# Kernel tuning notes

Hardware: AMD Instinct MI355X
Metric: run time of the kernel (lower is better)

The kernel has to match this reference:

```python
import jax, jax.numpy as jnp
import numpy as np

IN_F = 128
OUT_F = 128
SCALE = float(np.sqrt(OUT_F))

def swish(x):
    return x * jax.nn.sigmoid(x)

def setup_inputs() -> dict:
    key = jax.random.key(0)
    ks = jax.random.split(key, 10)
    B, A = 4, 4096
    s = 1.0 / np.sqrt(IN_F)
    return {
        "x": jax.random.normal(ks[0], (B, A, IN_F), dtype=jnp.float32),
        "connectivity": jax.random.normal(ks[1], (B, A, A), dtype=jnp.float32),
        "Wq": jax.random.uniform(ks[2], (IN_F, OUT_F), jnp.float32, -s, s),
        "Wk": jax.random.uniform(ks[3], (IN_F, OUT_F), jnp.float32, -s, s),
        "Wv": jax.random.uniform(ks[4], (IN_F, OUT_F), jnp.float32, -s, s),
        "W1": jax.random.uniform(ks[5], (OUT_F, OUT_F), jnp.float32, -s, s),
        "b1": jnp.zeros((OUT_F,), jnp.float32),
        "W2": jax.random.uniform(ks[6], (OUT_F, OUT_F), jnp.float32, -s, s),
        "b2": jnp.zeros((OUT_F,), jnp.float32),
        "gamma": jnp.ones((OUT_F,), jnp.float32),
        "beta": jnp.zeros((OUT_F,), jnp.float32),
    }

def reference(x, connectivity, Wq, Wk, Wv, W1, b1, W2, b2, gamma, beta):
    # Q,K,V projections (no bias): [B,A,D]
    Q = jnp.einsum('bah,hd->bad', x, Wq)
    K = jnp.einsum('bah,hd->bad', x, Wk)
    V = jnp.einsum('bah,hd->bad', x, Wv)
    # dense all-pairs scores with additive connectivity bias: [B,A,A]
    scores = jnp.einsum('bqd,bkd->bqk', Q, K) / SCALE + connectivity
    alpha = jax.nn.softmax(scores, axis=-1)
    # dropout p=0.0 / eval mode -> identity
    H = jnp.einsum('bqk,bkd->bqd', alpha, V)
    # Swish-MLP tail
    h = swish(H)
    h = h @ W1 + b1
    h = swish(h)
    h = h @ W2 + b2
    # LayerNorm over last dim (eps=1e-5 as torch default)
    mu = jnp.mean(h, axis=-1, keepdims=True)
    var = jnp.var(h, axis=-1, keepdims=True)
    return (h - mu) * jax.lax.rsqrt(var + 1e-5) * gamma + beta
```

## Files before the change

### kernel.cpp

```cpp
#include <hip/hip_runtime.h>

#define L2E 1.44269504088896340736f
#define INV_SCALE 0.08838834764831845f

typedef _Float16 half8 __attribute__((ext_vector_type(8)));
typedef _Float16 half4 __attribute__((ext_vector_type(4)));
typedef float f32x4 __attribute__((ext_vector_type(4)));

__device__ __forceinline__ float exp2_fast(float x) {
#if __has_builtin(__builtin_amdgcn_exp2f)
  return __builtin_amdgcn_exp2f(x);
#else
  return exp2f(x);
#endif
}

__device__ __forceinline__ f32x4 mfma16(half8 a, half8 b, f32x4 c) {
  return __builtin_amdgcn_mfma_f32_16x16x32_f16(a, b, c, 0, 0, 0);
}

__device__ __forceinline__ void gload16(const void* g, void* l) {
  __builtin_amdgcn_global_load_lds(
      (const __attribute__((address_space(1))) void*)g,
      (__attribute__((address_space(3))) void*)l, 16, 0, 0);
}

__device__ __forceinline__ float swish_f(float v) {
  return v / (1.f + exp2_fast(-L2E * v));
}

template <int CTRL>
__device__ __forceinline__ float dppmov(float x) {
  int xi = __builtin_bit_cast(int, x);
  int r = __builtin_amdgcn_update_dpp(xi, xi, CTRL, 0xf, 0xf, false);
  return __builtin_bit_cast(float, r);
}
__device__ __forceinline__ float red16_sum(float x) {
  x += dppmov<0xB1>(x);
  x += dppmov<0x4E>(x);
  x += dppmov<0x141>(x);
  x += dppmov<0x140>(x);
  return x;
}

__global__ __launch_bounds__(256) void prep_kernel(
    const float* __restrict__ Wq, const float* __restrict__ Wk,
    const float* __restrict__ Wv, const float* __restrict__ W1,
    const float* __restrict__ W2, _Float16* __restrict__ Wf) {
  const int g = blockIdx.x * 256 + threadIdx.x;
  const int mat = g >> 11, rem = g & 2047;
  const int f = rem >> 6, lane = rem & 63;
  const int n = (f >> 2) * 16 + (lane & 15);
  const int k0 = (f & 3) * 32 + (lane >> 4) * 8;
  const float* W = (mat == 0) ? Wq : (mat == 1) ? Wk : (mat == 2) ? Wv
                   : (mat == 3) ? W1 : W2;
  half8 h;
#pragma unroll
  for (int j = 0; j < 8; ++j) h[j] = (_Float16)W[(k0 + j) * 128 + n];
  *(half8*)(Wf + (size_t)g * 8) = h;
}

__global__ __launch_bounds__(256) void kv_kernel(
    const float* __restrict__ x, const _Float16* __restrict__ Wf,
    _Float16* __restrict__ Kg, _Float16* __restrict__ Vg) {
  __shared__ __align__(16) _Float16 sc[64 * 136];
  const int tid = threadIdx.x;
  const int w = tid >> 6, lane = tid & 63;
  const int n16 = lane & 15, quad = lane >> 4;
  const int blk = blockIdx.x;

  half8 xf[4];
  {
    const float* xr = x + (size_t)(blk * 64 + w * 16 + n16) * 128 + quad * 8;
#pragma unroll
    for (int kc = 0; kc < 4; ++kc) {
      float4 a = *(const float4*)(xr + kc * 32);
      float4 b = *(const float4*)(xr + kc * 32 + 4);
      half8 h;
      h[0] = (_Float16)a.x; h[1] = (_Float16)a.y;
      h[2] = (_Float16)a.z; h[3] = (_Float16)a.w;
      h[4] = (_Float16)b.x; h[5] = (_Float16)b.y;
      h[6] = (_Float16)b.z; h[7] = (_Float16)b.w;
      xf[kc] = h;
    }
  }

  for (int mat = 0; mat < 2; ++mat) {
    f32x4 acc[8];
#pragma unroll
    for (int ct = 0; ct < 8; ++ct) acc[ct] = f32x4{0.f, 0.f, 0.f, 0.f};
#pragma unroll
    for (int ct = 0; ct < 8; ++ct)
#pragma unroll
      for (int kc = 0; kc < 4; ++kc) {
        half8 wf = *(const half8*)(Wf +
            ((size_t)((mat + 1) * 32 + ct * 4 + kc) * 64 + lane) * 8);
        acc[ct] = mfma16(xf[kc], wf, acc[ct]);
      }
#pragma unroll
    for (int ct = 0; ct < 8; ++ct)
#pragma unroll
      for (int r = 0; r < 4; ++r)
        sc[(w * 16 + quad * 4 + r) * 136 + ct * 16 + n16] = (_Float16)acc[ct][r];
    __syncthreads();

    if (mat == 0) {
#pragma unroll
      for (int i = 0; i < 4; ++i) {
        const int c = tid + 256 * i;
        const int ln = c & 63, kc = (c >> 6) & 3, ct = (c >> 8) & 1, tl = (c >> 9) & 1;
        half8 v = *(const half8*)&sc[(tl * 32 + ct * 16 + (ln & 15)) * 136 +
                                     kc * 32 + (ln >> 4) * 8];
        *(half8*)(Kg + ((((size_t)(blk * 2 + tl)) * 2 + ct) * 4 + kc) * 512 + ln * 8) = v;
      }
    } else {
#pragma unroll
      for (int i = 0; i < 4; ++i) {
        const int c = tid + 256 * i;
        const int ln = c & 63, dt = (c >> 6) & 7, tl = (c >> 9) & 1;
        const int q2 = ln >> 4, nn = ln & 15;
        half8 v;
#pragma unroll
        for (int j = 0; j < 8; ++j)
          v[j] = sc[(tl * 32 + q2 * 8 + j) * 136 + dt * 16 + nn];
        *(half8*)(Vg + (((size_t)(blk * 2 + tl)) * 8 + dt) * 512 + ln * 8) = v;
      }
    }
    __syncthreads();
  }
}

__global__ __launch_bounds__(128) void flash_kernel(
    const float* __restrict__ x, const float* __restrict__ conn,
    const _Float16* __restrict__ Wf,
    const _Float16* __restrict__ Kg, const _Float16* __restrict__ Vg,
    _Float16* __restrict__ Og, float2* __restrict__ Ml,
    int nsplit, int nt) {
  __shared__ __align__(16) _Float16 kb[2][4096];
  __shared__ __align__(16) _Float16 vb[2][4096];
  __shared__ __align__(16) _Float16 pb[2][656];
  __shared__ __align__(16) float alb[2][16];

  const int tid = threadIdx.x, w = tid >> 6, lane = tid & 63;
  const int n16 = lane & 15, quad = lane >> 4;
  const int bid = blockIdx.x;
  int batch, sk, rg;
  if (nsplit == 2) {
    batch = bid & 3; sk = (bid >> 2) & 1; rg = bid >> 3;
  } else {
    batch = bid & 3; sk = 0; rg = bid >> 2;
  }
  const int rt_g = batch * 256 + rg * 2 + w;
  const int t0 = sk * nt;

  half8 qf[4];
  {
    half8 xf[4];
    const float* xr = x + (size_t)(batch * 4096 + rg * 32 + w * 16 + n16) * 128 + quad * 8;
#pragma unroll
    for (int kc = 0; kc < 4; ++kc) {
      float4 a = *(const float4*)(xr + kc * 32);
      float4 b = *(const float4*)(xr + kc * 32 + 4);
      half8 h;
      h[0] = (_Float16)a.x; h[1] = (_Float16)a.y;
      h[2] = (_Float16)a.z; h[3] = (_Float16)a.w;
      h[4] = (_Float16)b.x; h[5] = (_Float16)b.y;
      h[6] = (_Float16)b.z; h[7] = (_Float16)b.w;
      xf[kc] = h;
    }
    _Float16* tw = &kb[w][0];
#pragma unroll
    for (int ct = 0; ct < 8; ++ct) {
      f32x4 aq = f32x4{0.f, 0.f, 0.f, 0.f};
#pragma unroll
      for (int kc = 0; kc < 4; ++kc) {
        half8 wf = *(const half8*)(Wf + ((size_t)(ct * 4 + kc) * 64 + lane) * 8);
        aq = mfma16(xf[kc], wf, aq);
      }
#pragma unroll
      for (int r = 0; r < 4; ++r)
        tw[(quad * 4 + r) * 136 + ct * 16 + n16] = (_Float16)aq[r];
    }
#pragma unroll
    for (int kc = 0; kc < 4; ++kc)
      qf[kc] = *(const half8*)(tw + n16 * 136 + kc * 32 + quad * 8);
  }
  __syncthreads();

  const _Float16* kp = Kg + (size_t)batch * 524288 + (size_t)t0 * 4096 + tid * 8;
  const _Float16* vp = Vg + (size_t)batch * 524288 + (size_t)t0 * 4096 + tid * 8;
  const float* cp = conn + (size_t)batch * 16777216 +
                    (size_t)(rg * 32 + w * 16 + n16) * 4096 +
                    (size_t)t0 * 32 + quad * 4;
  const int wbase = (tid & ~63) * 8;

  auto stage = [&](int t, int buf) {
    const _Float16* ks = kp + (size_t)t * 4096;
    const _Float16* vs = vp + (size_t)t * 4096;
#pragma unroll
    for (int c = 0; c < 4; ++c) {
      gload16(ks + c * 1024, &kb[buf][c * 1024 + wbase]);
      gload16(vs + c * 1024, &vb[buf][c * 1024 + wbase]);
    }
  };
  auto ldconn = [&](int i, float4* cr) {
    const float* c0 = cp + (size_t)i * 32;
    cr[0] = *(const float4*)c0;
    cr[1] = *(const float4*)(c0 + 16);
  };

  f32x4 o[8];
#pragma unroll
  for (int dt = 0; dt < 8; ++dt) o[dt] = f32x4{0.f, 0.f, 0.f, 0.f};
  float m_i = -__builtin_inff();
  float l_i = 0.f;

  float4 ca[2], cb[2];
  stage(0, 0);
  ldconn(0, ca);
  __syncthreads();

  auto compute = [&](int buf, const float4* cc) {
    f32x4 s0 = f32x4{0.f, 0.f, 0.f, 0.f};
    f32x4 s1 = f32x4{0.f, 0.f, 0.f, 0.f};
    const _Float16* kc_ = kb[buf];
#pragma unroll
    for (int kc = 0; kc < 4; ++kc) {
      half8 kf0 = *(const half8*)&kc_[kc * 512 + lane * 8];
      half8 kf1 = *(const half8*)&kc_[(4 + kc) * 512 + lane * 8];
      s0 = mfma16(kf0, qf[kc], s0);
      s1 = mfma16(kf1, qf[kc], s1);
    }
    float pr[8];
#pragma unroll
    for (int r = 0; r < 4; ++r) {
      pr[r] = fmaf(s0[r], INV_SCALE, cc[0][r]);
      pr[4 + r] = fmaf(s1[r], INV_SCALE, cc[1][r]);
    }
    float mx = pr[0];
#pragma unroll
    for (int c = 1; c < 8; ++c) mx = fmaxf(mx, pr[c]);
    mx = fmaxf(mx, __shfl_xor(mx, 16, 64));
    mx = fmaxf(mx, __shfl_xor(mx, 32, 64));
    if (__any(mx > m_i)) {
      const float mn = fmaxf(m_i, mx);
      const float al = exp2_fast((m_i - mn) * L2E);
      m_i = mn;
      l_i *= al;
      if (quad == 0) alb[w][n16] = al;
      const float4 av = *(const float4*)&alb[w][quad * 4];
#pragma unroll
      for (int dt = 0; dt < 8; ++dt)
#pragma unroll
        for (int r = 0; r < 4; ++r) o[dt][r] *= av[r];
    }
    const float nm = -m_i * L2E;
#pragma unroll
    for (int c = 0; c < 8; ++c) pr[c] = exp2_fast(fmaf(pr[c], L2E, nm));
    float sm = pr[0];
#pragma unroll
    for (int c = 1; c < 8; ++c) sm += pr[c];
    sm += __shfl_xor(sm, 16, 64);
    sm += __shfl_xor(sm, 32, 64);
    l_i += sm;
    _Float16* pw = pb[w];
    half4 p0, p1;
#pragma unroll
    for (int r = 0; r < 4; ++r) {
      p0[r] = (_Float16)pr[r];
      p1[r] = (_Float16)pr[4 + r];
    }
    *(half4*)(pw + n16 * 40 + quad * 4) = p0;
    *(half4*)(pw + n16 * 40 + 16 + quad * 4) = p1;
    half8 pf = *(const half8*)(pw + n16 * 40 + quad * 8);
    const _Float16* vc = vb[buf];
#pragma unroll
    for (int dt = 0; dt < 8; ++dt) {
      half8 vf = *(const half8*)&vc[dt * 512 + lane * 8];
      o[dt] = mfma16(pf, vf, o[dt]);
    }
  };

#pragma unroll 1
  for (int i = 0; i < nt; i += 2) {
    stage(i + 1, 1);
    ldconn(i + 1, cb);
    compute(0, ca);
    __syncthreads();
    if (i + 2 < nt) {
      stage(i + 2, 0);
      ldconn(i + 2, ca);
    }
    compute(1, cb);
    __syncthreads();
  }

  if (quad == 0) alb[w][n16] = l_i;
  const float4 lv = *(const float4*)&alb[w][quad * 4];
  float il[4];
#pragma unroll
  for (int r = 0; r < 4; ++r) il[r] = 1.f / lv[r];
  _Float16* tw = &kb[w][0];
#pragma unroll
  for (int dt = 0; dt < 8; ++dt)
#pragma unroll
    for (int r = 0; r < 4; ++r)
      tw[(quad * 4 + r) * 136 + dt * 16 + n16] = (_Float16)(o[dt][r] * il[r]);
  _Float16* ob = Og + ((size_t)(sk * 1024 + rt_g) * 4) * 512;
#pragma unroll
  for (int kc = 0; kc < 4; ++kc) {
    half8 of = *(const half8*)(tw + n16 * 136 + kc * 32 + quad * 8);
    *(half8*)(ob + kc * 512 + lane * 8) = of;
  }
  if (quad == 0)
    Ml[sk * 16384 + rt_g * 16 + n16] = make_float2(m_i, l_i);
}

__global__ __launch_bounds__(256) void mlp_kernel(
    const _Float16* __restrict__ Og, const float2* __restrict__ Ml,
    const _Float16* __restrict__ Wf,
    const float* __restrict__ b1, const float* __restrict__ b2,
    const float* __restrict__ gamma, const float* __restrict__ beta,
    float* __restrict__ out, int nsplit) {
  __shared__ __align__(16) _Float16 hb[4][2176];
  const int tid = threadIdx.x, w = tid >> 6, lane = tid & 63;
  const int n16 = lane & 15, quad = lane >> 4;
  const int rt_g = blockIdx.x * 4 + w;

  float2 ml[2];
  float m = -__builtin_inff();
  for (int s = 0; s < nsplit; ++s) {
    ml[s] = Ml[s * 16384 + rt_g * 16 + n16];
    m = fmaxf(m, ml[s].x);
  }
  float wgt[2], wsum = 0.f;
  for (int s = 0; s < nsplit; ++s) {
    wgt[s] = ml[s].y * exp2_fast((ml[s].x - m) * L2E);
    wsum += wgt[s];
  }
  const float inv = 1.f / wsum;

  half8 hf[4];
#pragma unroll
  for (int kc = 0; kc < 4; ++kc) {
    float hv[8] = {0, 0, 0, 0, 0, 0, 0, 0};
    for (int s = 0; s < nsplit; ++s) {
      half8 ofr = *(const half8*)(Og +
          ((size_t)(s * 1024 + rt_g) * 4 + kc) * 512 + lane * 8);
#pragma unroll
      for (int j = 0; j < 8; ++j) hv[j] += wgt[s] * (float)ofr[j];
    }
    half8 h;
#pragma unroll
    for (int j = 0; j < 8; ++j) h[j] = (_Float16)swish_f(hv[j] * inv);
    hf[kc] = h;
  }

  float b1v[8], b2v[8], gv[8], bv[8];
#pragma unroll
  for (int ct = 0; ct < 8; ++ct) {
    b1v[ct] = b1[ct * 16 + n16];
    b2v[ct] = b2[ct * 16 + n16];
    gv[ct] = gamma[ct * 16 + n16];
    bv[ct] = beta[ct * 16 + n16];
  }

  f32x4 acc[8];
#pragma unroll
  for (int ct = 0; ct < 8; ++ct) acc[ct] = f32x4{0.f, 0.f, 0.f, 0.f};
#pragma unroll
  for (int ct = 0; ct < 8; ++ct)
#pragma unroll
    for (int kc = 0; kc < 4; ++kc) {
      half8 wf = *(const half8*)(Wf +
          ((size_t)(3 * 32 + ct * 4 + kc) * 64 + lane) * 8);
      acc[ct] = mfma16(hf[kc], wf, acc[ct]);
    }
  _Float16* hw = hb[w];
#pragma unroll
  for (int ct = 0; ct < 8; ++ct)
#pragma unroll
    for (int r = 0; r < 4; ++r)
      hw[(quad * 4 + r) * 136 + ct * 16 + n16] =
          (_Float16)swish_f(acc[ct][r] + b1v[ct]);
  half8 h1f[4];
#pragma unroll
  for (int kc = 0; kc < 4; ++kc)
    h1f[kc] = *(const half8*)(hw + n16 * 136 + kc * 32 + quad * 8);

#pragma unroll
  for (int ct = 0; ct < 8; ++ct) acc[ct] = f32x4{0.f, 0.f, 0.f, 0.f};
#pragma unroll
  for (int ct = 0; ct < 8; ++ct)
#pragma unroll
    for (int kc = 0; kc < 4; ++kc) {
      half8 wf = *(const half8*)(Wf +
          ((size_t)(4 * 32 + ct * 4 + kc) * 64 + lane) * 8);
      acc[ct] = mfma16(h1f[kc], wf, acc[ct]);
    }
  float hx[8][4];
  float sm[4] = {0, 0, 0, 0}, ss[4] = {0, 0, 0, 0};
#pragma unroll
  for (int ct = 0; ct < 8; ++ct)
#pragma unroll
    for (int r = 0; r < 4; ++r) {
      const float v = acc[ct][r] + b2v[ct];
      hx[ct][r] = v;
      sm[r] += v;
      ss[r] += v * v;
    }
#pragma unroll
  for (int r = 0; r < 4; ++r) {
    sm[r] = red16_sum(sm[r]);
    ss[r] = red16_sum(ss[r]);
  }
#pragma unroll
  for (int r = 0; r < 4; ++r) {
    const float mu = sm[r] * (1.f / 128.f);
    const float var = ss[r] * (1.f / 128.f) - mu * mu;
    const float rstd = rsqrtf(var + 1e-5f);
    const size_t row = (size_t)rt_g * 16 + quad * 4 + r;
#pragma unroll
    for (int ct = 0; ct < 8; ++ct)
      out[row * 128 + ct * 16 + n16] = (hx[ct][r] - mu) * rstd * gv[ct] + bv[ct];
  }
}

extern "C" void kernel_launch(void* const* d_in, const int* in_sizes, int n_in,
                              void* d_out, int out_size, void* d_ws,
                              size_t ws_size, hipStream_t stream) {
  const float* x     = (const float*)d_in[0];
  const float* conn  = (const float*)d_in[1];
  const float* Wq    = (const float*)d_in[2];
  const float* Wk    = (const float*)d_in[3];
  const float* Wv    = (const float*)d_in[4];
  const float* W1    = (const float*)d_in[5];
  const float* b1    = (const float*)d_in[6];
  const float* W2    = (const float*)d_in[7];
  const float* b2    = (const float*)d_in[8];
  const float* gamma = (const float*)d_in[9];
  const float* beta  = (const float*)d_in[10];
  float* out = (float*)d_out;

  const size_t need2 =
      ((size_t)81920 + 4 * 2097152) * 2 + 2 * 16384 * sizeof(float2);
  const int nsplit = (ws_size >= need2) ? 2 : 1;
  const int nt = 128 / nsplit;

  _Float16* Wf = (_Float16*)d_ws;
  _Float16* Kg = Wf + 81920;
  _Float16* Vg = Kg + 2097152;
  _Float16* Og = Vg + 2097152;
  float2* Ml = (float2*)(Og + (size_t)2097152 * nsplit);

  prep_kernel<<<40, 256, 0, stream>>>(Wq, Wk, Wv, W1, W2, Wf);
  kv_kernel<<<256, 256, 0, stream>>>(x, Wf, Kg, Vg);
  flash_kernel<<<512 * nsplit, 128, 0, stream>>>(x, conn, Wf, Kg, Vg, Og, Ml,
                                                 nsplit, nt);
  mlp_kernel<<<256, 256, 0, stream>>>(Og, Ml, Wf, b1, b2, gamma, beta, out,
                                      nsplit);
}
```

Baseline: 459.8 us.

## Template flash kernel on wave count, use four-wave blocks with four-way KV split

The flash attention kernel is templated on the number of waves per block. With enough workspace it launches 4-wave (256-thread) blocks that cover 64 query rows and share each staged K/V tile, and splits the key range four ways. Each K/V tile loaded into LDS is now reused by twice as many rows, cutting redundant K/V traffic per row, while the four-way split keeps the grid at 1024 blocks. The cost is more partial output written to workspace and merged in the MLP kernel, plus larger blocks that may lower occupancy.

```diff
diff --git a/kernel.cpp b/kernel.cpp
--- a/kernel.cpp
+++ b/kernel.cpp
@@ -130,7 +130,8 @@
   }
 }
 
-__global__ __launch_bounds__(128) void flash_kernel(
+template <int NW>
+__global__ __launch_bounds__(NW * 64) void flash_kernel(
     const float* __restrict__ x, const float* __restrict__ conn,
     const _Float16* __restrict__ Wf,
     const _Float16* __restrict__ Kg, const _Float16* __restrict__ Vg,
@@ -138,25 +139,30 @@
     int nsplit, int nt) {
   __shared__ __align__(16) _Float16 kb[2][4096];
   __shared__ __align__(16) _Float16 vb[2][4096];
-  __shared__ __align__(16) _Float16 pb[2][656];
-  __shared__ __align__(16) float alb[2][16];
+  __shared__ __align__(16) _Float16 pb[NW][656];
+  __shared__ __align__(16) float alb[NW][16];
 
   const int tid = threadIdx.x, w = tid >> 6, lane = tid & 63;
   const int n16 = lane & 15, quad = lane >> 4;
   const int bid = blockIdx.x;
   int batch, sk, rg;
-  if (nsplit == 2) {
+  if (nsplit == 4) {
+    batch = bid & 3; sk = (bid >> 2) & 3; rg = bid >> 4;
+  } else if (nsplit == 2) {
     batch = bid & 3; sk = (bid >> 2) & 1; rg = bid >> 3;
   } else {
     batch = bid & 3; sk = 0; rg = bid >> 2;
   }
-  const int rt_g = batch * 256 + rg * 2 + w;
+  const int rt_g = batch * 256 + rg * NW + w;
   const int t0 = sk * nt;
+  const int rowb = rg * (NW * 16) + w * 16 + n16;
+
+  _Float16* scratch = (w < 2) ? &kb[w][0] : &vb[w - 2][0];
 
   half8 qf[4];
   {
     half8 xf[4];
-    const float* xr = x + (size_t)(batch * 4096 + rg * 32 + w * 16 + n16) * 128 + quad * 8;
+    const float* xr = x + ((size_t)batch * 4096 + rowb) * 128 + quad * 8;
 #pragma unroll
     for (int kc = 0; kc < 4; ++kc) {
       float4 a = *(const float4*)(xr + kc * 32);
@@ -168,7 +174,7 @@
       h[6] = (_Float16)b.z; h[7] = (_Float16)b.w;
       xf[kc] = h;
     }
-    _Float16* tw = &kb[w][0];
+    _Float16* tw = scratch;
 #pragma unroll
     for (int ct = 0; ct < 8; ++ct) {
       f32x4 aq = f32x4{0.f, 0.f, 0.f, 0.f};
@@ -189,18 +195,18 @@
 
   const _Float16* kp = Kg + (size_t)batch * 524288 + (size_t)t0 * 4096 + tid * 8;
   const _Float16* vp = Vg + (size_t)batch * 524288 + (size_t)t0 * 4096 + tid * 8;
-  const float* cp = conn + (size_t)batch * 16777216 +
-                    (size_t)(rg * 32 + w * 16 + n16) * 4096 +
+  const float* cp = conn + (size_t)batch * 16777216 + (size_t)rowb * 4096 +
                     (size_t)t0 * 32 + quad * 4;
   const int wbase = (tid & ~63) * 8;
+  constexpr int NC = 8 / NW;
 
   auto stage = [&](int t, int buf) {
     const _Float16* ks = kp + (size_t)t * 4096;
     const _Float16* vs = vp + (size_t)t * 4096;
 #pragma unroll
-    for (int c = 0; c < 4; ++c) {
-      gload16(ks + c * 1024, &kb[buf][c * 1024 + wbase]);
-      gload16(vs + c * 1024, &vb[buf][c * 1024 + wbase]);
+    for (int c = 0; c < NC; ++c) {
+      gload16(ks + c * (NW * 512), &kb[buf][c * (NW * 512) + wbase]);
+      gload16(vs + c * (NW * 512), &vb[buf][c * (NW * 512) + wbase]);
     }
   };
   auto ldconn = [&](int i, float4* cr) {
@@ -300,7 +306,7 @@
   float il[4];
 #pragma unroll
   for (int r = 0; r < 4; ++r) il[r] = 1.f / lv[r];
-  _Float16* tw = &kb[w][0];
+  _Float16* tw = scratch;
 #pragma unroll
   for (int dt = 0; dt < 8; ++dt)
 #pragma unroll
@@ -327,13 +333,13 @@
   const int n16 = lane & 15, quad = lane >> 4;
   const int rt_g = blockIdx.x * 4 + w;
 
-  float2 ml[2];
+  float2 ml[4];
   float m = -__builtin_inff();
   for (int s = 0; s < nsplit; ++s) {
     ml[s] = Ml[s * 16384 + rt_g * 16 + n16];
     m = fmaxf(m, ml[s].x);
   }
-  float wgt[2], wsum = 0.f;
+  float wgt[4], wsum = 0.f;
   for (int s = 0; s < nsplit; ++s) {
     wgt[s] = ml[s].y * exp2_fast((ml[s].x - m) * L2E);
     wsum += wgt[s];
@@ -442,9 +448,12 @@
   const float* beta  = (const float*)d_in[10];
   float* out = (float*)d_out;
 
+  const size_t baseElems = (size_t)81920 + 2 * 2097152;
+  const size_t need4 =
+      (baseElems + 4 * 2097152) * 2 + 4 * 16384 * sizeof(float2);
   const size_t need2 =
-      ((size_t)81920 + 4 * 2097152) * 2 + 2 * 16384 * sizeof(float2);
-  const int nsplit = (ws_size >= need2) ? 2 : 1;
+      (baseElems + 2 * 2097152) * 2 + 2 * 16384 * sizeof(float2);
+  const int nsplit = (ws_size >= need4) ? 4 : (ws_size >= need2) ? 2 : 1;
   const int nt = 128 / nsplit;
 
   _Float16* Wf = (_Float16*)d_ws;
@@ -455,8 +464,16 @@
 
   prep_kernel<<<40, 256, 0, stream>>>(Wq, Wk, Wv, W1, W2, Wf);
   kv_kernel<<<256, 256, 0, stream>>>(x, Wf, Kg, Vg);
-  flash_kernel<<<512 * nsplit, 128, 0, stream>>>(x, conn, Wf, Kg, Vg, Og, Ml,
-                                                 nsplit, nt);
+  if (nsplit == 4) {
+    flash_kernel<4><<<1024, 256, 0, stream>>>(x, conn, Wf, Kg, Vg, Og, Ml,
+                                              nsplit, nt);
+  } else if (nsplit == 2) {
+    flash_kernel<2><<<1024, 128, 0, stream>>>(x, conn, Wf, Kg, Vg, Og, Ml,
+                                              nsplit, nt);
+  } else {
+    flash_kernel<2><<<512, 128, 0, stream>>>(x, conn, Wf, Kg, Vg, Og, Ml,
+                                             nsplit, nt);
+  }
   mlp_kernel<<<256, 256, 0, stream>>>(Og, Ml, Wf, b1, b2, gamma, beta, out,
                                       nsplit);
 }
```

New measurement: 475.0 us. 1.03x slower.

## Load K/V fragments directly into registers with single-wave flash blocks

Applied to the files above, without the earlier changes.

The flash kernel now runs one wave per block and loads K and V MFMA fragments straight from global memory into registers, double-buffering K across tiles. This drops the LDS staging and the block-wide barriers. The online-softmax rescale is also made lazy, firing only when the running max grows by more than 4. In exchange, each wave fetches its own K/V with no sharing between the two row tiles, so global/L2 traffic doubles, and register pressure rises.

```diff
diff --git a/kernel.cpp b/kernel.cpp
--- a/kernel.cpp
+++ b/kernel.cpp
@@ -17,12 +17,6 @@
 
 __device__ __forceinline__ f32x4 mfma16(half8 a, half8 b, f32x4 c) {
   return __builtin_amdgcn_mfma_f32_16x16x32_f16(a, b, c, 0, 0, 0);
-}
-
-__device__ __forceinline__ void gload16(const void* g, void* l) {
-  __builtin_amdgcn_global_load_lds(
-      (const __attribute__((address_space(1))) void*)g,
-      (__attribute__((address_space(3))) void*)l, 16, 0, 0);
 }
 
 __device__ __forceinline__ float swish_f(float v) {
@@ -130,18 +124,17 @@
   }
 }
 
-__global__ __launch_bounds__(128) void flash_kernel(
+__global__ __launch_bounds__(64, 2) void flash_kernel(
     const float* __restrict__ x, const float* __restrict__ conn,
     const _Float16* __restrict__ Wf,
     const _Float16* __restrict__ Kg, const _Float16* __restrict__ Vg,
     _Float16* __restrict__ Og, float2* __restrict__ Ml,
     int nsplit, int nt) {
-  __shared__ __align__(16) _Float16 kb[2][4096];
-  __shared__ __align__(16) _Float16 vb[2][4096];
-  __shared__ __align__(16) _Float16 pb[2][656];
-  __shared__ __align__(16) float alb[2][16];
-
-  const int tid = threadIdx.x, w = tid >> 6, lane = tid & 63;
+  __shared__ __align__(16) _Float16 scr[2176];
+  __shared__ __align__(16) _Float16 pb[656];
+  __shared__ __align__(16) float alb[16];
+
+  const int lane = threadIdx.x;
   const int n16 = lane & 15, quad = lane >> 4;
   const int bid = blockIdx.x;
   int batch, sk, rg;
@@ -150,13 +143,41 @@
   } else {
     batch = bid & 3; sk = 0; rg = bid >> 2;
   }
-  const int rt_g = batch * 256 + rg * 2 + w;
+  const int rt_g = batch * 256 + rg;
   const int t0 = sk * nt;
+  const int rowb = rg * 16 + n16;
+
+  const _Float16* kp = Kg + (size_t)batch * 524288 + (size_t)t0 * 4096;
+  const _Float16* vp = Vg + (size_t)batch * 524288 + (size_t)t0 * 4096;
+  const float* cp = conn + (size_t)batch * 16777216 + (size_t)rowb * 4096 +
+                    (size_t)t0 * 32 + quad * 4;
+
+  auto ldk = [&](int t, half8* kf) {
+#pragma unroll
+    for (int f = 0; f < 8; ++f)
+      kf[f] = *(const half8*)(kp + (size_t)t * 4096 + f * 512 + lane * 8);
+  };
+  auto ldv = [&](int t, half8* vf) {
+#pragma unroll
+    for (int f = 0; f < 8; ++f)
+      vf[f] = *(const half8*)(vp + (size_t)t * 4096 + f * 512 + lane * 8);
+  };
+  auto ldconn = [&](int i, float4* cr) {
+    const float* c0 = cp + (size_t)i * 32;
+    cr[0] = *(const float4*)c0;
+    cr[1] = *(const float4*)(c0 + 16);
+  };
+
+  half8 kfA[8], kfB[8], vf[8];
+  float4 ca[2], cb[2];
+  ldk(0, kfA);
+  ldconn(0, ca);
+  ldconn(1, cb);
 
   half8 qf[4];
   {
     half8 xf[4];
-    const float* xr = x + (size_t)(batch * 4096 + rg * 32 + w * 16 + n16) * 128 + quad * 8;
+    const float* xr = x + ((size_t)batch * 4096 + rowb) * 128 + quad * 8;
 #pragma unroll
     for (int kc = 0; kc < 4; ++kc) {
       float4 a = *(const float4*)(xr + kc * 32);
@@ -168,7 +189,6 @@
       h[6] = (_Float16)b.z; h[7] = (_Float16)b.w;
       xf[kc] = h;
     }
-    _Float16* tw = &kb[w][0];
 #pragma unroll
     for (int ct = 0; ct < 8; ++ct) {
       f32x4 aq = f32x4{0.f, 0.f, 0.f, 0.f};
@@ -179,35 +199,12 @@
       }
 #pragma unroll
       for (int r = 0; r < 4; ++r)
-        tw[(quad * 4 + r) * 136 + ct * 16 + n16] = (_Float16)aq[r];
+        scr[(quad * 4 + r) * 136 + ct * 16 + n16] = (_Float16)aq[r];
     }
 #pragma unroll
     for (int kc = 0; kc < 4; ++kc)
-      qf[kc] = *(const half8*)(tw + n16 * 136 + kc * 32 + quad * 8);
-  }
-  __syncthreads();
-
-  const _Float16* kp = Kg + (size_t)batch * 524288 + (size_t)t0 * 4096 + tid * 8;
-  const _Float16* vp = Vg + (size_t)batch * 524288 + (size_t)t0 * 4096 + tid * 8;
-  const float* cp = conn + (size_t)batch * 16777216 +
-                    (size_t)(rg * 32 + w * 16 + n16) * 4096 +
-                    (size_t)t0 * 32 + quad * 4;
-  const int wbase = (tid & ~63) * 8;
-
-  auto stage = [&](int t, int buf) {
-    const _Float16* ks = kp + (size_t)t * 4096;
-    const _Float16* vs = vp + (size_t)t * 4096;
-#pragma unroll
-    for (int c = 0; c < 4; ++c) {
-      gload16(ks + c * 1024, &kb[buf][c * 1024 + wbase]);
-      gload16(vs + c * 1024, &vb[buf][c * 1024 + wbase]);
-    }
-  };
-  auto ldconn = [&](int i, float4* cr) {
-    const float* c0 = cp + (size_t)i * 32;
-    cr[0] = *(const float4*)c0;
-    cr[1] = *(const float4*)(c0 + 16);
-  };
+      qf[kc] = *(const half8*)(scr + n16 * 136 + kc * 32 + quad * 8);
+  }
 
   f32x4 o[8];
 #pragma unroll
@@ -215,21 +212,13 @@
   float m_i = -__builtin_inff();
   float l_i = 0.f;
 
-  float4 ca[2], cb[2];
-  stage(0, 0);
-  ldconn(0, ca);
-  __syncthreads();
-
-  auto compute = [&](int buf, const float4* cc) {
+  auto tile = [&](const half8* kf, const float4* cc) {
     f32x4 s0 = f32x4{0.f, 0.f, 0.f, 0.f};
     f32x4 s1 = f32x4{0.f, 0.f, 0.f, 0.f};
-    const _Float16* kc_ = kb[buf];
 #pragma unroll
     for (int kc = 0; kc < 4; ++kc) {
-      half8 kf0 = *(const half8*)&kc_[kc * 512 + lane * 8];
-      half8 kf1 = *(const half8*)&kc_[(4 + kc) * 512 + lane * 8];
-      s0 = mfma16(kf0, qf[kc], s0);
-      s1 = mfma16(kf1, qf[kc], s1);
+      s0 = mfma16(kf[kc], qf[kc], s0);
+      s1 = mfma16(kf[4 + kc], qf[kc], s1);
     }
     float pr[8];
 #pragma unroll
@@ -242,13 +231,13 @@
     for (int c = 1; c < 8; ++c) mx = fmaxf(mx, pr[c]);
     mx = fmaxf(mx, __shfl_xor(mx, 16, 64));
     mx = fmaxf(mx, __shfl_xor(mx, 32, 64));
-    if (__any(mx > m_i)) {
+    if (__any(mx > m_i + 4.f)) {
       const float mn = fmaxf(m_i, mx);
       const float al = exp2_fast((m_i - mn) * L2E);
       m_i = mn;
       l_i *= al;
-      if (quad == 0) alb[w][n16] = al;
-      const float4 av = *(const float4*)&alb[w][quad * 4];
+      if (quad == 0) alb[n16] = al;
+      const float4 av = *(const float4*)&alb[quad * 4];
 #pragma unroll
       for (int dt = 0; dt < 8; ++dt)
 #pragma unroll
@@ -263,53 +252,47 @@
     sm += __shfl_xor(sm, 16, 64);
     sm += __shfl_xor(sm, 32, 64);
     l_i += sm;
-    _Float16* pw = pb[w];
     half4 p0, p1;
 #pragma unroll
     for (int r = 0; r < 4; ++r) {
       p0[r] = (_Float16)pr[r];
       p1[r] = (_Float16)pr[4 + r];
     }
-    *(half4*)(pw + n16 * 40 + quad * 4) = p0;
-    *(half4*)(pw + n16 * 40 + 16 + quad * 4) = p1;
-    half8 pf = *(const half8*)(pw + n16 * 40 + quad * 8);
-    const _Float16* vc = vb[buf];
-#pragma unroll
-    for (int dt = 0; dt < 8; ++dt) {
-      half8 vf = *(const half8*)&vc[dt * 512 + lane * 8];
-      o[dt] = mfma16(pf, vf, o[dt]);
-    }
+    *(half4*)(pb + n16 * 40 + quad * 4) = p0;
+    *(half4*)(pb + n16 * 40 + 16 + quad * 4) = p1;
+    half8 pf = *(const half8*)(pb + n16 * 40 + quad * 8);
+#pragma unroll
+    for (int dt = 0; dt < 8; ++dt) o[dt] = mfma16(pf, vf[dt], o[dt]);
   };
 
 #pragma unroll 1
-  for (int i = 0; i < nt; i += 2) {
-    stage(i + 1, 1);
-    ldconn(i + 1, cb);
-    compute(0, ca);
-    __syncthreads();
-    if (i + 2 < nt) {
-      stage(i + 2, 0);
-      ldconn(i + 2, ca);
-    }
-    compute(1, cb);
-    __syncthreads();
-  }
-
-  if (quad == 0) alb[w][n16] = l_i;
-  const float4 lv = *(const float4*)&alb[w][quad * 4];
+  for (int t = 0; t < nt; t += 2) {
+    ldv(t, vf);
+    if (t + 1 < nt) ldk(t + 1, kfB);
+    tile(kfA, ca);
+    if (t + 2 < nt) {
+      ldconn(t + 2, ca);
+      ldk(t + 2, kfA);
+    }
+    ldv(t + 1, vf);
+    tile(kfB, cb);
+    if (t + 3 < nt) ldconn(t + 3, cb);
+  }
+
+  if (quad == 0) alb[n16] = l_i;
+  const float4 lv = *(const float4*)&alb[quad * 4];
   float il[4];
 #pragma unroll
   for (int r = 0; r < 4; ++r) il[r] = 1.f / lv[r];
-  _Float16* tw = &kb[w][0];
 #pragma unroll
   for (int dt = 0; dt < 8; ++dt)
 #pragma unroll
     for (int r = 0; r < 4; ++r)
-      tw[(quad * 4 + r) * 136 + dt * 16 + n16] = (_Float16)(o[dt][r] * il[r]);
+      scr[(quad * 4 + r) * 136 + dt * 16 + n16] = (_Float16)(o[dt][r] * il[r]);
   _Float16* ob = Og + ((size_t)(sk * 1024 + rt_g) * 4) * 512;
 #pragma unroll
   for (int kc = 0; kc < 4; ++kc) {
-    half8 of = *(const half8*)(tw + n16 * 136 + kc * 32 + quad * 8);
+    half8 of = *(const half8*)(scr + n16 * 136 + kc * 32 + quad * 8);
     *(half8*)(ob + kc * 512 + lane * 8) = of;
   }
   if (quad == 0)
@@ -455,7 +438,7 @@
 
   prep_kernel<<<40, 256, 0, stream>>>(Wq, Wk, Wv, W1, W2, Wf);
   kv_kernel<<<256, 256, 0, stream>>>(x, Wf, Kg, Vg);
-  flash_kernel<<<512 * nsplit, 128, 0, stream>>>(x, conn, Wf, Kg, Vg, Og, Ml,
+  flash_kernel<<<1024 * nsplit, 64, 0, stream>>>(x, conn, Wf, Kg, Vg, Og, Ml,
                                                  nsplit, nt);
   mlp_kernel<<<256, 256, 0, stream>>>(Og, Ml, Wf, b1, b2, gamma, beta, out,
                                       nsplit);
```

After: 501.0 us. +9.0%, slower.
